# Kernel optimization log

Measured on AMD Instinct MI355X. Metric: run time of the kernel, lower is better.

## Reference

```python
import jax, jax.numpy as jnp
import numpy as np

B, D, K = 32768, 256, 1024


def setup_inputs() -> dict:
    key = jax.random.key(0)
    k1, k2 = jax.random.split(key)
    embedding = jax.random.normal(k1, (B, D), dtype=jnp.float32)
    codebook = jax.random.normal(k2, (K, D), dtype=jnp.float32)
    return {"embedding": embedding, "codebook": codebook}


def reference(embedding, codebook):
    # code_norms: (K,) squared L2 norm of each code
    code_norms = jnp.sum(codebook ** 2, axis=1)            # (K,)
    dots = embedding @ codebook.T                           # (B, K)
    alpha = dots / code_norms[None, :]                      # (B, K)
    # error for projecting e onto line of code c:
    #   ||e - alpha c||^2 = ||e||^2 - dots^2 / ||c||^2
    # (identical math to materializing (B,K,D) diff, without the blowup)
    e_norms = jnp.sum(embedding ** 2, axis=1, keepdims=True)  # (B, 1)
    errors = e_norms - dots ** 2 / code_norms[None, :]        # (B, K)
    indices = jnp.argmin(errors, axis=1)                      # (B,)
    # gather chosen projection: alpha[b, idx[b]] * codebook[idx[b]]
    alpha_sel = jnp.take_along_axis(alpha, indices[:, None], axis=1)  # (B, 1)
    z_out = alpha_sel * codebook[indices]                     # (B, D)
    return (z_out, indices)
```

## Files before the change

kernel.cpp:

```cpp
#include <hip/hip_runtime.h>
#include <cstdint>

#define B_ROWS 32768
#define DIM    256
#define KCODES 1024
#define NSPLIT 2

typedef _Float16 f16x8 __attribute__((ext_vector_type(8)));
typedef float    f32x4 __attribute__((ext_vector_type(4)));


__global__ __launch_bounds__(64) void vq_prep(const float* __restrict__ cb,
                                              _Float16* __restrict__ hi,
                                              _Float16* __restrict__ lo,
                                              float* __restrict__ inv_norm) {
  const int k = blockIdx.x;
  const int lane = threadIdx.x;
  float4 c = reinterpret_cast<const float4*>(cb)[k * 64 + lane];
  float nrm = c.x * c.x + c.y * c.y + c.z * c.z + c.w * c.w;
#pragma unroll
  for (int off = 32; off; off >>= 1) nrm += __shfl_xor(nrm, off);
  if (lane == 0) inv_norm[k] = 1.0f / nrm;

  float f[4] = {c.x, c.y, c.z, c.w};
  _Float16 h[4], l[4];
#pragma unroll
  for (int i = 0; i < 4; ++i) {
    h[i] = (_Float16)f[i];
    l[i] = (_Float16)((f[i] - (float)h[i]) * 2048.0f);
  }
  const int phys = (lane >> 1) ^ (k & 15);
  const int byteoff = k * 512 + phys * 16 + (lane & 1) * 8;
  *reinterpret_cast<uint2*>((char*)hi + byteoff) = *reinterpret_cast<uint2*>(h);
  *reinterpret_cast<uint2*>((char*)lo + byteoff) = *reinterpret_cast<uint2*>(l);
}

__device__ __forceinline__ void gld16(const void* g, void* l) {
  __builtin_amdgcn_global_load_lds(
      (const __attribute__((address_space(1))) uint32_t*)g,
      (__attribute__((address_space(3))) uint32_t*)l, 16, 0, 0);
}

__global__ __launch_bounds__(256, 2) void vq_main(const float* __restrict__ emb,
                                                  const _Float16* __restrict__ cbh,
                                                  const _Float16* __restrict__ cbl,
                                                  const float* __restrict__ inv_g,
                                                  float2* __restrict__ cand) {
  __shared__ uint4 Btile[2][1024];
  __shared__ float inv_s[KCODES];

  const int flat = threadIdx.x;
  const int wave = flat >> 6;
  const int lane = flat & 63;
  const int quad = lane >> 4;
  const int lr   = lane & 15;

  const int split  = blockIdx.x & (NSPLIT - 1);
  const int rowblk = blockIdx.x >> 1;
  const int t0 = split * 32;

  reinterpret_cast<float4*>(inv_s)[flat] = reinterpret_cast<const float4*>(inv_g)[flat];

  f16x8 Ah[2][8], Al[2][8];
  const int row0 = rowblk * 128 + wave * 32;
#pragma unroll
  for (int s = 0; s < 2; ++s) {
    const float* rp = emb + (size_t)(row0 + s * 16 + lr) * DIM;
#pragma unroll
    for (int c = 0; c < 8; ++c) {
      const float* p = rp + c * 32 + quad * 8;
      float4 f0 = *reinterpret_cast<const float4*>(p);
      float4 f1 = *reinterpret_cast<const float4*>(p + 4);
      float f[8] = {f0.x, f0.y, f0.z, f0.w, f1.x, f1.y, f1.z, f1.w};
      f16x8 h, l;
#pragma unroll
      for (int j = 0; j < 8; ++j) {
        _Float16 hv = (_Float16)f[j];
        h[j] = hv;
        l[j] = (_Float16)((f[j] - (float)hv) * 2048.0f);
      }
      Ah[s][c] = h;
      Al[s][c] = l;
    }
  }

  auto stage = [&](int buf, int t) {
    const char* srcH = (const char*)cbh + t * 8192;
    const char* srcL = (const char*)cbl + t * 8192;
    char* dst = (char*)&Btile[buf][0];
    const int off = flat * 16;
    gld16(srcH + off,        dst + off);
    gld16(srcH + 4096 + off, dst + 4096 + off);
    gld16(srcL + off,        dst + 8192 + off);
    gld16(srcL + 4096 + off, dst + 12288 + off);
  };
  stage(0, t0);

  float bg[2][4], bd[2][4];
  int   bk[2][4];
#pragma unroll
  for (int s = 0; s < 2; ++s)
#pragma unroll
    for (int r = 0; r < 4; ++r) { bg[s][r] = -1.0f; bd[s][r] = 0.0f; bk[s][r] = t0 * 16; }

  for (int t = t0; t < t0 + 32; ++t) {
    __syncthreads();
    if (t + 1 < t0 + 32) stage((t + 1) & 1, t + 1);
    const char* buf = (const char*)&Btile[t & 1][0];

    f32x4 accA0 = {0, 0, 0, 0}, accB0 = {0, 0, 0, 0};
    f32x4 accA1 = {0, 0, 0, 0}, accB1 = {0, 0, 0, 0};
#pragma unroll
    for (int c = 0; c < 8; ++c) {
      const int g = (((c * 4 + quad) ^ lr) * 16) + lr * 512;
      f16x8 bh = *reinterpret_cast<const f16x8*>(buf + g);
      f16x8 bl = *reinterpret_cast<const f16x8*>(buf + 8192 + g);
      accA0 = __builtin_amdgcn_mfma_f32_16x16x32_f16(Ah[0][c], bh, accA0, 0, 0, 0);
      accA1 = __builtin_amdgcn_mfma_f32_16x16x32_f16(Ah[1][c], bh, accA1, 0, 0, 0);
      accB0 = __builtin_amdgcn_mfma_f32_16x16x32_f16(Al[0][c], bh, accB0, 0, 0, 0);
      accB1 = __builtin_amdgcn_mfma_f32_16x16x32_f16(Al[1][c], bh, accB1, 0, 0, 0);
      accB0 = __builtin_amdgcn_mfma_f32_16x16x32_f16(Ah[0][c], bl, accB0, 0, 0, 0);
      accB1 = __builtin_amdgcn_mfma_f32_16x16x32_f16(Ah[1][c], bl, accB1, 0, 0, 0);
    }

    const int n = t * 16 + lr;
    const float inl = inv_s[n];
#pragma unroll
    for (int r = 0; r < 4; ++r) {
      float d0 = accA0[r] + accB0[r] * 4.8828125e-4f;
      float g0 = d0 * d0 * inl;
      if (g0 > bg[0][r]) { bg[0][r] = g0; bd[0][r] = d0; bk[0][r] = n; }
      float d1 = accA1[r] + accB1[r] * 4.8828125e-4f;
      float g1 = d1 * d1 * inl;
      if (g1 > bg[1][r]) { bg[1][r] = g1; bd[1][r] = d1; bk[1][r] = n; }
    }
  }

#pragma unroll
  for (int s = 0; s < 2; ++s) {
#pragma unroll
    for (int r = 0; r < 4; ++r) {
      float g = bg[s][r]; int k = bk[s][r]; float d = bd[s][r];
#pragma unroll
      for (int m = 1; m < 16; m <<= 1) {
        float g2 = __shfl_xor(g, m);
        int   k2 = __shfl_xor(k, m);
        float d2 = __shfl_xor(d, m);
        if (g2 > g || (g2 == g && k2 < k)) { g = g2; k = k2; d = d2; }
      }
      if (lr == 0) {
        const int row = row0 + s * 16 + quad * 4 + r;
        cand[(size_t)split * B_ROWS + row] = make_float2(d, __int_as_float(k));
      }
    }
  }
}

__global__ __launch_bounds__(256) void vq_reduce(const float2* __restrict__ cand,
                                                 const float* __restrict__ inv_g,
                                                 const float* __restrict__ cb,
                                                 float* __restrict__ out) {
  const int wave = threadIdx.x >> 6;
  const int lane = threadIdx.x & 63;
  const int row = blockIdx.x * 4 + wave;

  float best_g = -1.0f, best_d = 0.0f;
  int best_k = 0;
#pragma unroll
  for (int s = 0; s < NSPLIT; ++s) {
    float2 c = cand[(size_t)s * B_ROWS + row];
    int k = __float_as_int(c.y);
    float g = c.x * c.x * inv_g[k];
    if (g > best_g || (g == best_g && k < best_k)) {
      best_g = g; best_d = c.x; best_k = k;
    }
  }
  const float alpha = best_d * inv_g[best_k];
  float4 c4 = reinterpret_cast<const float4*>(cb)[best_k * 64 + lane];
  float4 z = {alpha * c4.x, alpha * c4.y, alpha * c4.z, alpha * c4.w};
  reinterpret_cast<float4*>(out)[(size_t)row * 64 + lane] = z;
  if (lane == 0) out[(size_t)B_ROWS * DIM + row] = (float)best_k;
}

extern "C" void kernel_launch(void* const* d_in, const int* in_sizes, int n_in,
                              void* d_out, int out_size, void* d_ws, size_t ws_size,
                              hipStream_t stream) {
  const float* emb = (const float*)d_in[0];
  const float* cb  = (const float*)d_in[1];
  _Float16* cbh = (_Float16*)d_ws;
  _Float16* cbl = (_Float16*)((char*)d_ws + (512 << 10));
  float*    inv = (float*)((char*)d_ws + (1 << 20));
  float2*   cand = (float2*)((char*)d_ws + (1 << 20) + 4096);

  vq_prep<<<KCODES, 64, 0, stream>>>(cb, cbh, cbl, inv);
  vq_main<<<(B_ROWS / 128) * NSPLIT, 256, 0, stream>>>(emb, cbh, cbl, inv, cand);
  vq_reduce<<<B_ROWS / 4, 256, 0, stream>>>(cand, inv, cb, (float*)d_out);
}
```

Measured before the change: 139.6 us.

## Double row tile per wave and overlap epilogue with next tile's MFMAs

Each wave now holds 64 embedding rows (4 sub-tiles) instead of 32, so every codebook tile staged in LDS feeds twice as many MFMAs. The grid halves and launch bounds drop to one block per SM-equivalent. The loop is manually unrolled by two with separate accumulator sets, so the argmax epilogue of one tile runs interleaved with the MFMAs of the next. This raises register pressure sharply (A fragments plus double accumulators) and lowers occupancy, risking spills or worse latency hiding.

```diff
diff --git a/kernel.cpp b/kernel.cpp
--- a/kernel.cpp
+++ b/kernel.cpp
@@ -41,7 +41,7 @@
       (__attribute__((address_space(3))) uint32_t*)l, 16, 0, 0);
 }
 
-__global__ __launch_bounds__(256, 2) void vq_main(const float* __restrict__ emb,
+__global__ __launch_bounds__(256, 1) void vq_main(const float* __restrict__ emb,
                                                   const _Float16* __restrict__ cbh,
                                                   const _Float16* __restrict__ cbl,
                                                   const float* __restrict__ inv_g,
@@ -61,10 +61,10 @@
 
   reinterpret_cast<float4*>(inv_s)[flat] = reinterpret_cast<const float4*>(inv_g)[flat];
 
-  f16x8 Ah[2][8], Al[2][8];
-  const int row0 = rowblk * 128 + wave * 32;
-#pragma unroll
-  for (int s = 0; s < 2; ++s) {
+  f16x8 Ah[4][8], Al[4][8];
+  const int row0 = rowblk * 256 + wave * 64;
+#pragma unroll
+  for (int s = 0; s < 4; ++s) {
     const float* rp = emb + (size_t)(row0 + s * 16 + lr) * DIM;
 #pragma unroll
     for (int c = 0; c < 8; ++c) {
@@ -96,51 +96,64 @@
   };
   stage(0, t0);
 
-  float bg[2][4], bd[2][4];
-  int   bk[2][4];
-#pragma unroll
-  for (int s = 0; s < 2; ++s)
-#pragma unroll
-    for (int r = 0; r < 4; ++r) { bg[s][r] = -1.0f; bd[s][r] = 0.0f; bk[s][r] = t0 * 16; }
-
-  for (int t = t0; t < t0 + 32; ++t) {
-    __syncthreads();
-    if (t + 1 < t0 + 32) stage((t + 1) & 1, t + 1);
-    const char* buf = (const char*)&Btile[t & 1][0];
-
-    f32x4 accA0 = {0, 0, 0, 0}, accB0 = {0, 0, 0, 0};
-    f32x4 accA1 = {0, 0, 0, 0}, accB1 = {0, 0, 0, 0};
+  float bg[16], bd[16];
+  int   bk[16];
+#pragma unroll
+  for (int i = 0; i < 16; ++i) { bg[i] = -1.0f; bd[i] = 0.0f; bk[i] = t0 * 16; }
+
+  auto comp = [&](const char* buf, f32x4* aA, f32x4* aB) {
+#pragma unroll
+    for (int s = 0; s < 4; ++s) {
+      aA[s] = (f32x4){0, 0, 0, 0};
+      aB[s] = (f32x4){0, 0, 0, 0};
+    }
 #pragma unroll
     for (int c = 0; c < 8; ++c) {
       const int g = (((c * 4 + quad) ^ lr) * 16) + lr * 512;
       f16x8 bh = *reinterpret_cast<const f16x8*>(buf + g);
       f16x8 bl = *reinterpret_cast<const f16x8*>(buf + 8192 + g);
-      accA0 = __builtin_amdgcn_mfma_f32_16x16x32_f16(Ah[0][c], bh, accA0, 0, 0, 0);
-      accA1 = __builtin_amdgcn_mfma_f32_16x16x32_f16(Ah[1][c], bh, accA1, 0, 0, 0);
-      accB0 = __builtin_amdgcn_mfma_f32_16x16x32_f16(Al[0][c], bh, accB0, 0, 0, 0);
-      accB1 = __builtin_amdgcn_mfma_f32_16x16x32_f16(Al[1][c], bh, accB1, 0, 0, 0);
-      accB0 = __builtin_amdgcn_mfma_f32_16x16x32_f16(Ah[0][c], bl, accB0, 0, 0, 0);
-      accB1 = __builtin_amdgcn_mfma_f32_16x16x32_f16(Ah[1][c], bl, accB1, 0, 0, 0);
-    }
-
+#pragma unroll
+      for (int s = 0; s < 4; ++s) {
+        aA[s] = __builtin_amdgcn_mfma_f32_16x16x32_f16(Ah[s][c], bh, aA[s], 0, 0, 0);
+        aB[s] = __builtin_amdgcn_mfma_f32_16x16x32_f16(Al[s][c], bh, aB[s], 0, 0, 0);
+        aB[s] = __builtin_amdgcn_mfma_f32_16x16x32_f16(Ah[s][c], bl, aB[s], 0, 0, 0);
+      }
+    }
+  };
+
+  auto epi = [&](const f32x4* aA, const f32x4* aB, int t) {
     const int n = t * 16 + lr;
     const float inl = inv_s[n];
 #pragma unroll
+    for (int s = 0; s < 4; ++s)
+#pragma unroll
+      for (int r = 0; r < 4; ++r) {
+        float d = fmaf(aB[s][r], 4.8828125e-4f, aA[s][r]);
+        float g = d * d * inl;
+        const int i = (s << 2) | r;
+        if (g > bg[i]) { bg[i] = g; bd[i] = d; bk[i] = n; }
+      }
+  };
+
+  f32x4 aA0[4], aB0[4], aA1[4], aB1[4];
+  for (int tt = 0; tt < 32; tt += 2) {
+    __syncthreads();
+    stage(1, t0 + tt + 1);
+    comp((const char*)&Btile[0][0], aA0, aB0);
+    if (tt) epi(aA1, aB1, t0 + tt - 1);
+    __syncthreads();
+    if (tt + 2 < 32) stage(0, t0 + tt + 2);
+    comp((const char*)&Btile[1][0], aA1, aB1);
+    epi(aA0, aB0, t0 + tt);
+  }
+  epi(aA1, aB1, t0 + 31);
+
+#pragma unroll
+  for (int s = 0; s < 4; ++s) {
+#pragma unroll
     for (int r = 0; r < 4; ++r) {
-      float d0 = accA0[r] + accB0[r] * 4.8828125e-4f;
-      float g0 = d0 * d0 * inl;
-      if (g0 > bg[0][r]) { bg[0][r] = g0; bd[0][r] = d0; bk[0][r] = n; }
-      float d1 = accA1[r] + accB1[r] * 4.8828125e-4f;
-      float g1 = d1 * d1 * inl;
-      if (g1 > bg[1][r]) { bg[1][r] = g1; bd[1][r] = d1; bk[1][r] = n; }
-    }
-  }
-
-#pragma unroll
-  for (int s = 0; s < 2; ++s) {
-#pragma unroll
-    for (int r = 0; r < 4; ++r) {
-      float g = bg[s][r]; int k = bk[s][r]; float d = bd[s][r];
+      const int i = (s << 2) | r;
+      float g = bg[i]; int k = bk[i]; float d = bd[i];
 #pragma unroll
       for (int m = 1; m < 16; m <<= 1) {
         float g2 = __shfl_xor(g, m);
@@ -193,6 +206,6 @@
   float2*   cand = (float2*)((char*)d_ws + (1 << 20) + 4096);
 
   vq_prep<<<KCODES, 64, 0, stream>>>(cb, cbh, cbl, inv);
-  vq_main<<<(B_ROWS / 128) * NSPLIT, 256, 0, stream>>>(emb, cbh, cbl, inv, cand);
+  vq_main<<<(B_ROWS / 256) * NSPLIT, 256, 0, stream>>>(emb, cbh, cbl, inv, cand);
   vq_reduce<<<B_ROWS / 4, 256, 0, stream>>>(cand, inv, cb, (float*)d_out);
 }
```

Measured after the change: 158.3 us. 1.13x slower.
